# Performance work log

Hardware: AMD Instinct MI355X
Metric: run time of the kernel (lower is better)

## Reference

```python
import jax, jax.numpy as jnp
import numpy as np

K_BITS = 128  # hash bits (k in __init__)
WORD = 32     # pack bits into uint32 words -> K_BITS // WORD = 4 words


def _pack_bits(bits_u32):
    # bits_u32: [N, K_BITS] uint32 in {0,1} -> [N, K_BITS//WORD] uint32 keys
    N = bits_u32.shape[0]
    b = bits_u32.reshape(N, K_BITS // WORD, WORD)
    shifts = jnp.arange(WORD, dtype=jnp.uint32)
    return jnp.sum(jnp.left_shift(b, shifts), axis=-1, dtype=jnp.uint32)  # [N, 4]


def setup_inputs() -> dict:
    key = jax.random.key(0)
    k1, k2 = jax.random.split(key)
    T, B, D = 128, 64, 4096
    latent_state = jax.random.normal(k1, (T, B, D), dtype=jnp.float32)
    A = jax.random.normal(k2, (K_BITS, D), dtype=jnp.float32)  # fixed random projection buffer
    return {"latent_state": latent_state, "A": A}


def reference(latent_state, A):
    # latent_state: [T, B, D]; A: [k, D]. Returns intrinsic reward [T, B].
    T, B, D = latent_state.shape
    flat = latent_state.reshape(T * B, D)                    # detach is a no-op for fwd
    proj = flat @ A.T                                        # [N, k]
    bits = (proj > 0).astype(jnp.uint32)                     # SimHash sign bits
    words = _pack_bits(bits)                                 # [N, 4] collision-free 128-bit key

    # counts dict starts empty each run: visit count of row i is the number of
    # rows j <= i with an identical key (keys processed in row order).
    N = words.shape[0]
    eq = jnp.ones((N, N), dtype=bool)
    for w in range(K_BITS // WORD):  # small fixed loop over 4 key words
        eq = eq & (words[:, None, w] == words[None, :, w])
    counts = jnp.tril(eq).sum(axis=1)                        # [N] int, >= 1
    intrinsic = 1.0 / jnp.sqrt(counts.astype(latent_state.dtype))
    return intrinsic.reshape(T, B)
```

## Files before the change

### kernel.cpp

```cpp
#include <hip/hip_runtime.h>
#include <stdint.h>

#define D_DIM 4096
#define N_ROWS 8192

typedef __attribute__((ext_vector_type(8))) short bfrag8;
typedef __attribute__((ext_vector_type(4))) float facc4;
typedef unsigned long long u64;

__device__ __forceinline__ uint32_t pack_bf16x2(float lo, float hi) {
    union { float f; uint32_t u; } a, b;
    a.f = lo; b.f = hi;
    return (b.u & 0xFFFF0000u) | (a.u >> 16);
}

__global__ void __launch_bounds__(256)
prep_A(const float* __restrict__ A, uint32_t* __restrict__ Bimg) {
    const int S = blockIdx.x * 256 + threadIdx.x;
    const int chunk = S >> 10;
    const int rest  = S & 1023;
    const int tks   = rest >> 6;
    const int lane  = rest & 63;
    const int t  = tks >> 1;
    const int ks = tks & 1;
    const int c  = lane & 15;
    const int q  = lane >> 4;
    const float* src = A + (size_t)(16 * t + c) * D_DIM + chunk * 64 + ks * 32 + q * 8;
    float4 f0 = *(const float4*)(src);
    float4 f1 = *(const float4*)(src + 4);
    uint4 o;
    o.x = pack_bf16x2(f0.x, f0.y);
    o.y = pack_bf16x2(f0.z, f0.w);
    o.z = pack_bf16x2(f1.x, f1.y);
    o.w = pack_bf16x2(f1.z, f1.w);
    *(uint4*)(Bimg + (size_t)S * 4) = o;
}

__global__ void __launch_bounds__(256, 3)
gemm_direct(const float* __restrict__ L, const uint32_t* __restrict__ Bimg,
            float* __restrict__ partials, int kpb) {
    const int tid  = threadIdx.x;
    const int lane = tid & 63;
    const int gw   = blockIdx.x * 4 + (tid >> 6);
    const int split = gw >> 9;
    const int mwave = gw & 511;
    const int c = lane & 15;
    const int q = lane >> 4;

    const float* lrow = L + (size_t)(16 * mwave + c) * D_DIM;

    facc4 acc[8];
#pragma unroll
    for (int t = 0; t < 8; t++) acc[t] = (facc4){0.f, 0.f, 0.f, 0.f};

    const int k0 = split * kpb;
#pragma unroll 2
    for (int k = k0; k < k0 + kpb; k++) {
        const int kc = k * 64;
        bfrag8 a[2];
#pragma unroll
        for (int ks = 0; ks < 2; ks++) {
            const float* p = lrow + kc + ks * 32 + q * 8;
            float4 f0 = *(const float4*)(p);
            float4 f1 = *(const float4*)(p + 4);
            uint4 u;
            u.x = pack_bf16x2(f0.x, f0.y);
            u.y = pack_bf16x2(f0.z, f0.w);
            u.z = pack_bf16x2(f1.x, f1.y);
            u.w = pack_bf16x2(f1.z, f1.w);
            a[ks] = *(bfrag8*)&u;
        }
        const uint32_t* bbase = Bimg + ((size_t)k * 16) * 256 + lane * 4;
#pragma unroll
        for (int t = 0; t < 8; t++) {
#pragma unroll
            for (int ks = 0; ks < 2; ks++) {
                bfrag8 b = *(const bfrag8*)(bbase + (t * 2 + ks) * 256);
                acc[t] = __builtin_amdgcn_mfma_f32_16x16x32_bf16(a[ks], b, acc[t], 0, 0, 0);
            }
        }
    }

    float* P = partials + (size_t)split * N_ROWS * 128 + (size_t)(16 * mwave) * 128;
#pragma unroll
    for (int t = 0; t < 8; t++)
#pragma unroll
        for (int r = 0; r < 4; r++)
            P[(4 * q + r) * 128 + 16 * t + c] = acc[t][r];
}

__global__ void __launch_bounds__(256)
reduce_pack(const float* __restrict__ partials, u64* __restrict__ folded, int S) {
    const int row  = blockIdx.x * 4 + (threadIdx.x >> 6);
    const int lane = threadIdx.x & 63;
    float s0 = 0.f, s1 = 0.f;
    for (int s = 0; s < S; s++) {
        const float* P = partials + ((size_t)s * N_ROWS * 128) + (size_t)row * 128;
        s0 += P[lane];
        s1 += P[lane + 64];
    }
    u64 b0 = __ballot(s0 > 0.0f);
    u64 b1 = __ballot(s1 > 0.0f);
    if (lane == 0) folded[row] = b0 ^ b1;
}

__global__ void __launch_bounds__(256)
count_rows(const u64* __restrict__ folded, float* __restrict__ out) {
    __shared__ u64 K[N_ROWS];
    const int tid = threadIdx.x;
    for (int i = tid; i < N_ROWS / 2; i += 256)
        ((uint4*)K)[i] = ((const uint4*)folded)[i];
    __syncthreads();

    const int g    = blockIdx.x * 4 + (tid >> 6);
    const int lane = tid & 63;
    int rows[4];
    u64 my[4];
    int cnt[4] = {0, 0, 0, 0};
#pragma unroll
    for (int r = 0; r < 4; r++) {
        rows[r] = g + 2048 * r;
        my[r] = K[rows[r]];
    }
    const int maxrow = rows[3];
    for (int j = lane; j <= maxrow; j += 64) {
        u64 k = K[j];
#pragma unroll
        for (int r = 0; r < 4; r++)
            cnt[r] += (int)((j <= rows[r]) & (k == my[r]));
    }
#pragma unroll
    for (int r = 0; r < 4; r++) {
        int v = cnt[r];
#pragma unroll
        for (int o = 32; o; o >>= 1) v += __shfl_xor(v, o, 64);
        if (lane == 0) out[rows[r]] = rsqrtf((float)v);
    }
}

extern "C" void kernel_launch(void* const* d_in, const int* in_sizes, int n_in,
                              void* d_out, int out_size, void* d_ws, size_t ws_size,
                              hipStream_t stream) {
    const float* latent = (const float*)d_in[0];
    const float* A      = (const float*)d_in[1];
    float* out          = (float*)d_out;

    uint32_t* Bimg = (uint32_t*)d_ws;
    u64* folded = (u64*)((char*)d_ws + (1 << 20));
    float* partials = (float*)((char*)d_ws + (1 << 20) + (1 << 16));

    const size_t base = (1 << 20) + (1 << 16);
    const size_t per_split = (size_t)N_ROWS * 128 * sizeof(float);
    int S = 1;
    if (ws_size >= base + 8 * per_split)      S = 8;
    else if (ws_size >= base + 4 * per_split) S = 4;
    else if (ws_size >= base + 2 * per_split) S = 2;

    prep_A<<<256, 256, 0, stream>>>(A, Bimg);
    gemm_direct<<<128 * S, 256, 0, stream>>>(latent, Bimg, partials, 64 / S);
    reduce_pack<<<2048, 256, 0, stream>>>(partials, folded, S);
    count_rows<<<512, 256, 0, stream>>>(folded, out);
}
```

Before: 240.9 us.

## Pre-convert latent to bf16 MFMA fragment layout and reduce K-splits in LDS

Adds a prep_L kernel that converts the latent matrix to bf16 and stores it in MFMA-fragment order, staging through shared memory so both reads and writes are coalesced. A new gemm_frag kernel reads those fragments directly and splits K across the four waves of a block, summing three of the four wave results in LDS before writing only 4 partial sets. The aim is to replace the strided fp32 row loads and per-lane conversion in the GEMM. The cost is an extra 64 MB bf16 round-trip through global memory and a larger workspace requirement, with the old path kept as a fallback.

```diff
diff --git a/kernel.cpp b/kernel.cpp
--- a/kernel.cpp
+++ b/kernel.cpp
@@ -36,6 +36,138 @@
     *(uint4*)(Bimg + (size_t)S * 4) = o;
 }
 
+__global__ void __launch_bounds__(256)
+prep_L(const float* __restrict__ L, uint32_t* __restrict__ Aimg) {
+    __shared__ ushort T[16 * 528];
+    const int tid = threadIdx.x, w = tid >> 6, lane = tid & 63;
+    const int mw    = blockIdx.x >> 3;
+    const int kslab = blockIdx.x & 7;
+    const int k0 = kslab * 512;
+
+#pragma unroll
+    for (int rr = 0; rr < 4; rr++) {
+        const int r = 4 * w + rr;
+        const float* src = L + (size_t)(mw * 16 + r) * D_DIM + k0;
+#pragma unroll
+        for (int h = 0; h < 2; h++) {
+            float4 f = *(const float4*)(src + h * 256 + lane * 4);
+            uint2 u = make_uint2(pack_bf16x2(f.x, f.y), pack_bf16x2(f.z, f.w));
+            *(uint2*)&T[r * 528 + h * 256 + lane * 4] = u;
+        }
+    }
+    __syncthreads();
+
+    const int c = lane & 15, q = lane >> 4;
+#pragma unroll
+    for (int p = 0; p < 4; p++) {
+        const int cs  = 4 * w + p;
+        const int chl = cs >> 1, ks = cs & 1;
+        uint4 v = *(const uint4*)&T[c * 528 + chl * 64 + ks * 32 + q * 8];
+        const size_t G = ((size_t)mw * 128 + (size_t)(kslab * 8 + chl) * 2 + ks) * 64 + lane;
+        *(uint4*)(Aimg + G * 4) = v;
+    }
+}
+
+__global__ void __launch_bounds__(256)
+gemm_frag(const uint32_t* __restrict__ Aimg, const uint32_t* __restrict__ Bimg,
+          float* __restrict__ partials) {
+    __shared__ float red[3 * 2048];
+    const int tid = threadIdx.x, w = tid >> 6, lane = tid & 63;
+    const int outer = blockIdx.x;
+    const int mw    = blockIdx.y;
+    const int split = outer * 4 + w;
+    const int c = lane & 15, q = lane >> 4;
+
+    facc4 acc[8];
+#pragma unroll
+    for (int t = 0; t < 8; t++) acc[t] = (facc4){0.f, 0.f, 0.f, 0.f};
+
+#pragma unroll
+    for (int ch = 0; ch < 4; ch++) {
+        const int chunk = split * 4 + ch;
+        const uint32_t* ab = Aimg + (((size_t)mw * 128 + chunk * 2) * 64 + lane) * 4;
+        bfrag8 a0 = *(const bfrag8*)(ab);
+        bfrag8 a1 = *(const bfrag8*)(ab + 256);
+        const uint32_t* bb = Bimg + (size_t)chunk * 4096 + lane * 4;
+#pragma unroll
+        for (int t = 0; t < 8; t++) {
+            bfrag8 b0 = *(const bfrag8*)(bb + (t * 2 + 0) * 256);
+            acc[t] = __builtin_amdgcn_mfma_f32_16x16x32_bf16(a0, b0, acc[t], 0, 0, 0);
+            bfrag8 b1 = *(const bfrag8*)(bb + (t * 2 + 1) * 256);
+            acc[t] = __builtin_amdgcn_mfma_f32_16x16x32_bf16(a1, b1, acc[t], 0, 0, 0);
+        }
+    }
+
+    if (w) {
+        float* dst = red + (w - 1) * 2048;
+#pragma unroll
+        for (int t = 0; t < 8; t++)
+#pragma unroll
+            for (int r = 0; r < 4; r++)
+                dst[(4 * q + r) * 128 + 16 * t + c] = acc[t][r];
+    }
+    __syncthreads();
+    if (w == 0) {
+        float* P = partials + (size_t)outer * (N_ROWS * 128) + (size_t)(mw * 16) * 128;
+#pragma unroll
+        for (int t = 0; t < 8; t++)
+#pragma unroll
+            for (int r = 0; r < 4; r++) {
+                const int e = (4 * q + r) * 128 + 16 * t + c;
+                P[e] = acc[t][r] + red[e] + red[2048 + e] + red[4096 + e];
+            }
+    }
+}
+
+__global__ void __launch_bounds__(256)
+reduce_pack(const float* __restrict__ partials, u64* __restrict__ folded, int S) {
+    const int row  = blockIdx.x * 4 + (threadIdx.x >> 6);
+    const int lane = threadIdx.x & 63;
+    float s0 = 0.f, s1 = 0.f;
+    for (int s = 0; s < S; s++) {
+        const float* P = partials + ((size_t)s * N_ROWS * 128) + (size_t)row * 128;
+        s0 += P[lane];
+        s1 += P[lane + 64];
+    }
+    u64 b0 = __ballot(s0 > 0.0f);
+    u64 b1 = __ballot(s1 > 0.0f);
+    if (lane == 0) folded[row] = b0 ^ b1;
+}
+
+__global__ void __launch_bounds__(256)
+count_rows(const u64* __restrict__ folded, float* __restrict__ out) {
+    __shared__ u64 K[N_ROWS];
+    const int tid = threadIdx.x;
+    for (int i = tid; i < N_ROWS / 2; i += 256)
+        ((uint4*)K)[i] = ((const uint4*)folded)[i];
+    __syncthreads();
+
+    const int g    = blockIdx.x * 4 + (tid >> 6);
+    const int lane = tid & 63;
+    int rows[4];
+    u64 my[4];
+    int cnt[4] = {0, 0, 0, 0};
+#pragma unroll
+    for (int r = 0; r < 4; r++) {
+        rows[r] = g + 2048 * r;
+        my[r] = K[rows[r]];
+    }
+    const int maxrow = rows[3];
+    for (int j = lane; j <= maxrow; j += 64) {
+        u64 k = K[j];
+#pragma unroll
+        for (int r = 0; r < 4; r++)
+            cnt[r] += (int)((j <= rows[r]) & (k == my[r]));
+    }
+#pragma unroll
+    for (int r = 0; r < 4; r++) {
+        int v = cnt[r];
+#pragma unroll
+        for (int o = 32; o; o >>= 1) v += __shfl_xor(v, o, 64);
+        if (lane == 0) out[rows[r]] = rsqrtf((float)v);
+    }
+}
+
 __global__ void __launch_bounds__(256, 3)
 gemm_direct(const float* __restrict__ L, const uint32_t* __restrict__ Bimg,
             float* __restrict__ partials, int kpb) {
@@ -46,7 +178,6 @@
     const int mwave = gw & 511;
     const int c = lane & 15;
     const int q = lane >> 4;
-
     const float* lrow = L + (size_t)(16 * mwave + c) * D_DIM;
 
     facc4 acc[8];
@@ -80,62 +211,12 @@
             }
         }
     }
-
     float* P = partials + (size_t)split * N_ROWS * 128 + (size_t)(16 * mwave) * 128;
 #pragma unroll
     for (int t = 0; t < 8; t++)
 #pragma unroll
         for (int r = 0; r < 4; r++)
             P[(4 * q + r) * 128 + 16 * t + c] = acc[t][r];
-}
-
-__global__ void __launch_bounds__(256)
-reduce_pack(const float* __restrict__ partials, u64* __restrict__ folded, int S) {
-    const int row  = blockIdx.x * 4 + (threadIdx.x >> 6);
-    const int lane = threadIdx.x & 63;
-    float s0 = 0.f, s1 = 0.f;
-    for (int s = 0; s < S; s++) {
-        const float* P = partials + ((size_t)s * N_ROWS * 128) + (size_t)row * 128;
-        s0 += P[lane];
-        s1 += P[lane + 64];
-    }
-    u64 b0 = __ballot(s0 > 0.0f);
-    u64 b1 = __ballot(s1 > 0.0f);
-    if (lane == 0) folded[row] = b0 ^ b1;
-}
-
-__global__ void __launch_bounds__(256)
-count_rows(const u64* __restrict__ folded, float* __restrict__ out) {
-    __shared__ u64 K[N_ROWS];
-    const int tid = threadIdx.x;
-    for (int i = tid; i < N_ROWS / 2; i += 256)
-        ((uint4*)K)[i] = ((const uint4*)folded)[i];
-    __syncthreads();
-
-    const int g    = blockIdx.x * 4 + (tid >> 6);
-    const int lane = tid & 63;
-    int rows[4];
-    u64 my[4];
-    int cnt[4] = {0, 0, 0, 0};
-#pragma unroll
-    for (int r = 0; r < 4; r++) {
-        rows[r] = g + 2048 * r;
-        my[r] = K[rows[r]];
-    }
-    const int maxrow = rows[3];
-    for (int j = lane; j <= maxrow; j += 64) {
-        u64 k = K[j];
-#pragma unroll
-        for (int r = 0; r < 4; r++)
-            cnt[r] += (int)((j <= rows[r]) & (k == my[r]));
-    }
-#pragma unroll
-    for (int r = 0; r < 4; r++) {
-        int v = cnt[r];
-#pragma unroll
-        for (int o = 32; o; o >>= 1) v += __shfl_xor(v, o, 64);
-        if (lane == 0) out[rows[r]] = rsqrtf((float)v);
-    }
 }
 
 extern "C" void kernel_launch(void* const* d_in, const int* in_sizes, int n_in,
@@ -145,19 +226,31 @@
     const float* A      = (const float*)d_in[1];
     float* out          = (float*)d_out;
 
+    const size_t OFF_FOLDED = (size_t)1 << 20;
+    const size_t OFF_AIMG   = OFF_FOLDED + ((size_t)1 << 16);
+    const size_t OFF_PART   = OFF_AIMG + ((size_t)64 << 20);
+    const size_t NEED       = OFF_PART + ((size_t)16 << 20);
+
     uint32_t* Bimg = (uint32_t*)d_ws;
-    u64* folded = (u64*)((char*)d_ws + (1 << 20));
-    float* partials = (float*)((char*)d_ws + (1 << 20) + (1 << 16));
-
-    const size_t base = (1 << 20) + (1 << 16);
-    const size_t per_split = (size_t)N_ROWS * 128 * sizeof(float);
-    int S = 1;
-    if (ws_size >= base + 8 * per_split)      S = 8;
-    else if (ws_size >= base + 4 * per_split) S = 4;
-    else if (ws_size >= base + 2 * per_split) S = 2;
+    u64* folded    = (u64*)((char*)d_ws + OFF_FOLDED);
 
     prep_A<<<256, 256, 0, stream>>>(A, Bimg);
-    gemm_direct<<<128 * S, 256, 0, stream>>>(latent, Bimg, partials, 64 / S);
-    reduce_pack<<<2048, 256, 0, stream>>>(partials, folded, S);
+
+    if (ws_size >= NEED) {
+        uint32_t* Aimg  = (uint32_t*)((char*)d_ws + OFF_AIMG);
+        float* partials = (float*)((char*)d_ws + OFF_PART);
+        prep_L<<<4096, 256, 0, stream>>>(latent, Aimg);
+        gemm_frag<<<dim3(4, 512), 256, 0, stream>>>(Aimg, Bimg, partials);
+        reduce_pack<<<2048, 256, 0, stream>>>(partials, folded, 4);
+    } else {
+        float* partials = (float*)((char*)d_ws + OFF_AIMG);
+        const size_t per_split = (size_t)N_ROWS * 128 * sizeof(float);
+        int S = 1;
+        if (ws_size >= OFF_AIMG + 8 * per_split)      S = 8;
+        else if (ws_size >= OFF_AIMG + 4 * per_split) S = 4;
+        else if (ws_size >= OFF_AIMG + 2 * per_split) S = 2;
+        gemm_direct<<<128 * S, 256, 0, stream>>>(latent, Bimg, partials, 64 / S);
+        reduce_pack<<<2048, 256, 0, stream>>>(partials, folded, S);
+    }
     count_rows<<<512, 256, 0, stream>>>(folded, out);
 }
```

Measured after the change: 250.1 us. 3.8% more time.

## Switch GEMM to 32x32 MFMA tiles with in-block split-K reduction via LDS

Applied to the files above, without the earlier changes.

The projection GEMM now uses 32x32x16 bf16 MFMA instructions, and the A image is re-laid out to match. Each block covers 32 rows, and its four waves each take a different K range. The waves reduce their partial sums through shared memory before writing, so the split count is fixed at 4 and no longer depends on workspace size. The goal is fewer MFMA issues, fewer B-fragment loads per FLOP, and less partial-sum traffic to global memory. In exchange it adds 48KB of LDS per block, which limits occupancy, and a block-wide synchronisation.

```diff
diff --git a/kernel.cpp b/kernel.cpp
--- a/kernel.cpp
+++ b/kernel.cpp
@@ -5,7 +5,7 @@
 #define N_ROWS 8192
 
 typedef __attribute__((ext_vector_type(8))) short bfrag8;
-typedef __attribute__((ext_vector_type(4))) float facc4;
+typedef __attribute__((ext_vector_type(16))) float facc16;
 typedef unsigned long long u64;
 
 __device__ __forceinline__ uint32_t pack_bf16x2(float lo, float hi) {
@@ -17,15 +17,12 @@
 __global__ void __launch_bounds__(256)
 prep_A(const float* __restrict__ A, uint32_t* __restrict__ Bimg) {
     const int S = blockIdx.x * 256 + threadIdx.x;
-    const int chunk = S >> 10;
-    const int rest  = S & 1023;
-    const int tks   = rest >> 6;
-    const int lane  = rest & 63;
-    const int t  = tks >> 1;
-    const int ks = tks & 1;
-    const int c  = lane & 15;
-    const int q  = lane >> 4;
-    const float* src = A + (size_t)(16 * t + c) * D_DIM + chunk * 64 + ks * 32 + q * 8;
+    const int lane = S & 63;
+    const int g = S >> 6;
+    const int t = g & 3, ks = (g >> 2) & 3, chunk = g >> 4;
+    const int n  = 32 * t + (lane & 31);
+    const int k0 = chunk * 64 + ks * 16 + (lane >> 5) * 8;
+    const float* src = A + (size_t)n * D_DIM + k0;
     float4 f0 = *(const float4*)(src);
     float4 f1 = *(const float4*)(src + 4);
     uint4 o;
@@ -36,31 +33,33 @@
     *(uint4*)(Bimg + (size_t)S * 4) = o;
 }
 
-__global__ void __launch_bounds__(256, 3)
-gemm_direct(const float* __restrict__ L, const uint32_t* __restrict__ Bimg,
-            float* __restrict__ partials, int kpb) {
-    const int tid  = threadIdx.x;
-    const int lane = tid & 63;
-    const int gw   = blockIdx.x * 4 + (tid >> 6);
-    const int split = gw >> 9;
-    const int mwave = gw & 511;
-    const int c = lane & 15;
-    const int q = lane >> 4;
+__global__ void __launch_bounds__(256)
+gemm32(const float* __restrict__ L, const uint32_t* __restrict__ Bimg,
+       float* __restrict__ partials) {
+    __shared__ float red[3 * 4096];
+    const int tid = threadIdx.x, w = tid >> 6, lane = tid & 63;
+    const int outer = blockIdx.x;
+    const int mt    = blockIdx.y;
+    const int split = outer * 4 + w;
+    const int n31 = lane & 31, q8 = lane >> 5;
+    const int row0 = mt * 32;
 
-    const float* lrow = L + (size_t)(16 * mwave + c) * D_DIM;
+    const float* lrow = L + (size_t)(row0 + n31) * D_DIM + q8 * 8;
 
-    facc4 acc[8];
+    facc16 acc[4];
 #pragma unroll
-    for (int t = 0; t < 8; t++) acc[t] = (facc4){0.f, 0.f, 0.f, 0.f};
+    for (int t = 0; t < 4; t++)
+#pragma unroll
+        for (int r = 0; r < 16; r++) acc[t][r] = 0.0f;
 
-    const int k0 = split * kpb;
-#pragma unroll 2
-    for (int k = k0; k < k0 + kpb; k++) {
-        const int kc = k * 64;
-        bfrag8 a[2];
 #pragma unroll
-        for (int ks = 0; ks < 2; ks++) {
-            const float* p = lrow + kc + ks * 32 + q * 8;
+    for (int ch = 0; ch < 4; ch++) {
+        const int chunk = split * 4 + ch;
+        const int kc = chunk * 64;
+        bfrag8 a[4];
+#pragma unroll
+        for (int ks = 0; ks < 4; ks++) {
+            const float* p = lrow + kc + ks * 16;
             float4 f0 = *(const float4*)(p);
             float4 f1 = *(const float4*)(p + 4);
             uint4 u;
@@ -70,23 +69,38 @@
             u.w = pack_bf16x2(f1.z, f1.w);
             a[ks] = *(bfrag8*)&u;
         }
-        const uint32_t* bbase = Bimg + ((size_t)k * 16) * 256 + lane * 4;
+        const uint32_t* bb = Bimg + (size_t)chunk * 4096 + lane * 4;
 #pragma unroll
-        for (int t = 0; t < 8; t++) {
+        for (int ks = 0; ks < 4; ks++)
 #pragma unroll
-            for (int ks = 0; ks < 2; ks++) {
-                bfrag8 b = *(const bfrag8*)(bbase + (t * 2 + ks) * 256);
-                acc[t] = __builtin_amdgcn_mfma_f32_16x16x32_bf16(a[ks], b, acc[t], 0, 0, 0);
+            for (int t = 0; t < 4; t++) {
+                bfrag8 b = *(const bfrag8*)(bb + (ks * 4 + t) * 256);
+                acc[t] = __builtin_amdgcn_mfma_f32_32x32x16_bf16(a[ks], b, acc[t], 0, 0, 0);
             }
-        }
     }
 
-    float* P = partials + (size_t)split * N_ROWS * 128 + (size_t)(16 * mwave) * 128;
+    if (w) {
+        float* dst = red + (w - 1) * 4096;
 #pragma unroll
-    for (int t = 0; t < 8; t++)
+        for (int t = 0; t < 4; t++)
 #pragma unroll
-        for (int r = 0; r < 4; r++)
-            P[(4 * q + r) * 128 + 16 * t + c] = acc[t][r];
+            for (int r = 0; r < 16; r++) {
+                const int row_l = (r & 3) + 8 * (r >> 2) + 4 * q8;
+                dst[row_l * 128 + 32 * t + n31] = acc[t][r];
+            }
+    }
+    __syncthreads();
+    if (w == 0) {
+        float* P = partials + (size_t)outer * (N_ROWS * 128) + (size_t)row0 * 128;
+#pragma unroll
+        for (int t = 0; t < 4; t++)
+#pragma unroll
+            for (int r = 0; r < 16; r++) {
+                const int row_l = (r & 3) + 8 * (r >> 2) + 4 * q8;
+                const int e = row_l * 128 + 32 * t + n31;
+                P[e] = acc[t][r] + red[e] + red[4096 + e] + red[8192 + e];
+            }
+    }
 }
 
 __global__ void __launch_bounds__(256)
@@ -145,19 +159,12 @@
     const float* A      = (const float*)d_in[1];
     float* out          = (float*)d_out;
 
-    uint32_t* Bimg = (uint32_t*)d_ws;
-    u64* folded = (u64*)((char*)d_ws + (1 << 20));
+    uint32_t* Bimg  = (uint32_t*)d_ws;
+    u64* folded     = (u64*)((char*)d_ws + (1 << 20));
     float* partials = (float*)((char*)d_ws + (1 << 20) + (1 << 16));
 
-    const size_t base = (1 << 20) + (1 << 16);
-    const size_t per_split = (size_t)N_ROWS * 128 * sizeof(float);
-    int S = 1;
-    if (ws_size >= base + 8 * per_split)      S = 8;
-    else if (ws_size >= base + 4 * per_split) S = 4;
-    else if (ws_size >= base + 2 * per_split) S = 2;
-
     prep_A<<<256, 256, 0, stream>>>(A, Bimg);
-    gemm_direct<<<128 * S, 256, 0, stream>>>(latent, Bimg, partials, 64 / S);
-    reduce_pack<<<2048, 256, 0, stream>>>(partials, folded, S);
+    gemm32<<<dim3(4, 256), 256, 0, stream>>>(latent, Bimg, partials);
+    reduce_pack<<<2048, 256, 0, stream>>>(partials, folded, 4);
     count_rows<<<512, 256, 0, stream>>>(folded, out);
 }
```

New measurement: 230.5 us. -4.3%, faster.

## Fuse GEMM split-K reduction and bit packing, stage latent rows via LDS

Applied to the files above, without the earlier changes.

Replaces the split-K GEMM plus separate reduce kernel with one kernel per 16-row tile. Each of the four waves handles a quarter of K and double-buffers its latent slabs into padded LDS using global_load_lds. The waves then reduce their partial sums through shared memory, and the sign ballots are repacked into folded 64-bit keys in the same kernel. This removes the partials round trip through global memory and one kernel launch, in exchange for only 512 blocks and heavy LDS use that may limit occupancy.

```diff
diff --git a/kernel.cpp b/kernel.cpp
--- a/kernel.cpp
+++ b/kernel.cpp
@@ -3,6 +3,8 @@
 
 #define D_DIM 4096
 #define N_ROWS 8192
+#define ROW_STRIDE 1040
+#define SLAB_BYTES (16 * ROW_STRIDE)
 
 typedef __attribute__((ext_vector_type(8))) short bfrag8;
 typedef __attribute__((ext_vector_type(4))) float facc4;
@@ -36,72 +38,103 @@
     *(uint4*)(Bimg + (size_t)S * 4) = o;
 }
 
-__global__ void __launch_bounds__(256, 3)
-gemm_direct(const float* __restrict__ L, const uint32_t* __restrict__ Bimg,
-            float* __restrict__ partials, int kpb) {
-    const int tid  = threadIdx.x;
-    const int lane = tid & 63;
-    const int gw   = blockIdx.x * 4 + (tid >> 6);
-    const int split = gw >> 9;
-    const int mwave = gw & 511;
-    const int c = lane & 15;
-    const int q = lane >> 4;
+__global__ void __launch_bounds__(256)
+gemm_fused(const float* __restrict__ L, const uint32_t* __restrict__ Bimg,
+           u64* __restrict__ folded) {
+    __shared__ char sm[8 * SLAB_BYTES];
+    const int tid = threadIdx.x, w = tid >> 6, lane = tid & 63;
+    const int row0 = blockIdx.x * 16;
+    const int c = lane & 15, q = lane >> 4;
+    const int k0 = w * 1024;
 
-    const float* lrow = L + (size_t)(16 * mwave + c) * D_DIM;
+    char* buf0 = sm + (2 * w + 0) * SLAB_BYTES;
+    char* buf1 = sm + (2 * w + 1) * SLAB_BYTES;
+    const float* lbase = L + (size_t)row0 * D_DIM + k0;
+
+#define STAGE(sl, dstbuf)                                                        \
+    {                                                                            \
+        const float* _s = lbase + (sl) * 256;                                    \
+        _Pragma("unroll")                                                        \
+        for (int _r = 0; _r < 16; _r++)                                          \
+            __builtin_amdgcn_global_load_lds(                                    \
+                (const __attribute__((address_space(1))) uint32_t*)              \
+                    (_s + (size_t)_r * D_DIM + lane * 4),                        \
+                (__attribute__((address_space(3))) uint32_t*)                    \
+                    ((dstbuf) + _r * ROW_STRIDE),                                \
+                16, 0, 0);                                                       \
+    }
 
     facc4 acc[8];
 #pragma unroll
     for (int t = 0; t < 8; t++) acc[t] = (facc4){0.f, 0.f, 0.f, 0.f};
 
-    const int k0 = split * kpb;
-#pragma unroll 2
-    for (int k = k0; k < k0 + kpb; k++) {
-        const int kc = k * 64;
-        bfrag8 a[2];
+    STAGE(0, buf0);
 #pragma unroll
-        for (int ks = 0; ks < 2; ks++) {
-            const float* p = lrow + kc + ks * 32 + q * 8;
-            float4 f0 = *(const float4*)(p);
-            float4 f1 = *(const float4*)(p + 4);
-            uint4 u;
-            u.x = pack_bf16x2(f0.x, f0.y);
-            u.y = pack_bf16x2(f0.z, f0.w);
-            u.z = pack_bf16x2(f1.x, f1.y);
-            u.w = pack_bf16x2(f1.z, f1.w);
-            a[ks] = *(bfrag8*)&u;
-        }
-        const uint32_t* bbase = Bimg + ((size_t)k * 16) * 256 + lane * 4;
+    for (int sl = 0; sl < 4; sl++) {
+        if (sl == 0) STAGE(1, buf1);
+        if (sl == 1) STAGE(2, buf0);
+        if (sl == 2) STAGE(3, buf1);
+        if (sl < 3) __builtin_amdgcn_s_waitcnt(0x4F70);
+        else        __builtin_amdgcn_s_waitcnt(0x0F70);
+        const char* buf = (sl & 1) ? buf1 : buf0;
 #pragma unroll
-        for (int t = 0; t < 8; t++) {
+        for (int ch = 0; ch < 4; ch++) {
+            const int chunk = (w * 4 + sl) * 4 + ch;
 #pragma unroll
             for (int ks = 0; ks < 2; ks++) {
-                bfrag8 b = *(const bfrag8*)(bbase + (t * 2 + ks) * 256);
-                acc[t] = __builtin_amdgcn_mfma_f32_16x16x32_bf16(a[ks], b, acc[t], 0, 0, 0);
+                const char* ap = buf + c * ROW_STRIDE + ch * 256 + ks * 128 + q * 32;
+                float4 f0 = *(const float4*)(ap);
+                float4 f1 = *(const float4*)(ap + 16);
+                uint4 u;
+                u.x = pack_bf16x2(f0.x, f0.y);
+                u.y = pack_bf16x2(f0.z, f0.w);
+                u.z = pack_bf16x2(f1.x, f1.y);
+                u.w = pack_bf16x2(f1.z, f1.w);
+                bfrag8 a = *(bfrag8*)&u;
+                const uint32_t* bb = Bimg + ((size_t)(chunk * 16 + ks) * 64 + lane) * 4;
+#pragma unroll
+                for (int t = 0; t < 8; t++) {
+                    bfrag8 b = *(const bfrag8*)(bb + (size_t)t * 512);
+                    acc[t] = __builtin_amdgcn_mfma_f32_16x16x32_bf16(a, b, acc[t], 0, 0, 0);
+                }
             }
         }
     }
+#undef STAGE
 
-    float* P = partials + (size_t)split * N_ROWS * 128 + (size_t)(16 * mwave) * 128;
+    __syncthreads();
+    float* red = (float*)sm;
+    if (w) {
+        float* dst = red + (w - 1) * 2048;
 #pragma unroll
-    for (int t = 0; t < 8; t++)
+        for (int t = 0; t < 8; t++)
 #pragma unroll
-        for (int r = 0; r < 4; r++)
-            P[(4 * q + r) * 128 + 16 * t + c] = acc[t][r];
-}
-
-__global__ void __launch_bounds__(256)
-reduce_pack(const float* __restrict__ partials, u64* __restrict__ folded, int S) {
-    const int row  = blockIdx.x * 4 + (threadIdx.x >> 6);
-    const int lane = threadIdx.x & 63;
-    float s0 = 0.f, s1 = 0.f;
-    for (int s = 0; s < S; s++) {
-        const float* P = partials + ((size_t)s * N_ROWS * 128) + (size_t)row * 128;
-        s0 += P[lane];
-        s1 += P[lane + 64];
+            for (int r = 0; r < 4; r++)
+                dst[(4 * q + r) * 128 + 16 * t + c] = acc[t][r];
     }
-    u64 b0 = __ballot(s0 > 0.0f);
-    u64 b1 = __ballot(s1 > 0.0f);
-    if (lane == 0) folded[row] = b0 ^ b1;
+    __syncthreads();
+    if (w == 0) {
+        u64 masks[8][4];
+#pragma unroll
+        for (int t = 0; t < 8; t++)
+#pragma unroll
+            for (int r = 0; r < 4; r++) {
+                const int e = (4 * q + r) * 128 + 16 * t + c;
+                float v = acc[t][r] + red[e] + red[2048 + e] + red[4096 + e];
+                masks[t][r] = __ballot(v > 0.0f);
+            }
+        if (lane < 16) {
+            const int qq = lane >> 2, rr = lane & 3;
+            u64 h0 = 0, h1 = 0;
+#pragma unroll
+            for (int t = 0; t < 4; t++)
+                h0 |= (u64)((masks[t][rr] >> (16 * qq)) & 0xFFFFull) << (16 * t);
+#pragma unroll
+            for (int t = 4; t < 8; t++)
+                h1 |= (u64)((masks[t][rr] >> (16 * qq)) & 0xFFFFull) << (16 * (t - 4));
+            folded[row0 + lane] = h0 ^ h1;
+        }
+    }
 }
 
 __global__ void __launch_bounds__(256)
@@ -146,18 +179,9 @@
     float* out          = (float*)d_out;
 
     uint32_t* Bimg = (uint32_t*)d_ws;
-    u64* folded = (u64*)((char*)d_ws + (1 << 20));
-    float* partials = (float*)((char*)d_ws + (1 << 20) + (1 << 16));
-
-    const size_t base = (1 << 20) + (1 << 16);
-    const size_t per_split = (size_t)N_ROWS * 128 * sizeof(float);
-    int S = 1;
-    if (ws_size >= base + 8 * per_split)      S = 8;
-    else if (ws_size >= base + 4 * per_split) S = 4;
-    else if (ws_size >= base + 2 * per_split) S = 2;
+    u64* folded    = (u64*)((char*)d_ws + (1 << 20));
 
     prep_A<<<256, 256, 0, stream>>>(A, Bimg);
-    gemm_direct<<<128 * S, 256, 0, stream>>>(latent, Bimg, partials, 64 / S);
-    reduce_pack<<<2048, 256, 0, stream>>>(partials, folded, S);
+    gemm_fused<<<512, 256, 0, stream>>>(latent, Bimg, folded);
     count_rows<<<512, 256, 0, stream>>>(folded, out);
 }
```

Measured after the change: 252.5 us. 4.8% more time.
